# Performance work log

Measured on AMD Instinct MI355X. Metric: run time of the kernel, lower is better.

Reference implementation:

```python
import jax, jax.numpy as jnp
import numpy as np

B, S, H = 4, 2048, 1024
EXP_BITS, SIG_BITS = 5, 10  # rmode=1 -> round-to-nearest


def quantize(x):
    """Simulated low-precision float quantization (LightChop-style) with STE.

    exp_bits exponent bits (bias = 2^(e-1)-1, exponent clamped -> subnormal
    handling falls out of the clamp), sig_bits significand bits, round-to-nearest.
    """
    bias = 2 ** (EXP_BITS - 1) - 1
    ax = jnp.abs(x)
    e = jnp.floor(jnp.log2(jnp.where(ax > 0, ax, 1.0)))
    e = jnp.clip(e, 1 - bias, bias)               # clamp to representable exponent range
    scale = jnp.exp2(e - SIG_BITS)                # ulp at this exponent
    q = jnp.round(x / scale) * scale              # round significand to SIG_BITS bits
    max_val = (2.0 - 2.0 ** (-SIG_BITS)) * 2.0 ** bias
    q = jnp.clip(q, -max_val, max_val)            # saturate overflow
    # straight-through estimator: forward = q, backward = identity
    return x + jax.lax.stop_gradient(q - x)


def setup_inputs() -> dict:
    key = jax.random.key(0)
    ks = jax.random.split(key, 7)
    w_scale = 1.0 / np.sqrt(H)
    return {
        "x": jax.random.normal(ks[0], (B, S, H), dtype=jnp.float32),
        "Wq": jax.random.normal(ks[1], (H, H), dtype=jnp.float32) * w_scale,
        "bq": jax.random.normal(ks[2], (H,), dtype=jnp.float32) * 0.01,
        "Wk": jax.random.normal(ks[3], (H, H), dtype=jnp.float32) * w_scale,
        "bk": jax.random.normal(ks[4], (H,), dtype=jnp.float32) * 0.01,
        "Wv": jax.random.normal(ks[5], (H, H), dtype=jnp.float32) * w_scale,
        "bv": jax.random.normal(ks[6], (H,), dtype=jnp.float32) * 0.01,
    }


def reference(x, Wq, bq, Wk, bk, Wv, bv):
    # nn.Linear: y = x @ W.T + b   (W stored [out, in])
    q = quantize(jnp.einsum("bsh,oh->bso", x, Wq) + bq)
    k = quantize(jnp.einsum("bsh,oh->bso", x, Wk) + bk)
    v = quantize(jnp.einsum("bsh,oh->bso", x, Wv) + bv)
    inv_sqrt_h = 1.0 / (H ** 0.5)
    scores = quantize(jnp.einsum("bsh,bth->bst", q, k) * inv_sqrt_h)  # [B,S,S]
    attn = quantize(jax.nn.softmax(scores, axis=-1))
    return jnp.einsum("bst,bth->bsh", attn, v)
```

## Files before the change

kernel.cpp:

```cpp
#include <hip/hip_runtime.h>
#include <hip/hip_fp16.h>

#define B_ 4
#define S_ 2048
#define H_ 1024
#define M_ (B_ * S_)

typedef _Float16 f16;
typedef _Float16 f16x8 __attribute__((ext_vector_type(8)));
typedef _Float16 f16x4 __attribute__((ext_vector_type(4)));
typedef float f32x4 __attribute__((ext_vector_type(4)));

typedef __attribute__((address_space(3))) unsigned int* lds_u32p;
typedef const __attribute__((address_space(1))) unsigned int* gbl_u32p;

__device__ __forceinline__ void stage16(const f16* g, f16* l) {
  __builtin_amdgcn_global_load_lds((gbl_u32p)g, (lds_u32p)l, 16, 0, 0);
}

__global__ __launch_bounds__(256) void downconvert_all(
    const float* __restrict__ x, const float* __restrict__ W0,
    const float* __restrict__ W1, const float* __restrict__ W2,
    f16* __restrict__ xh, f16* __restrict__ Wh) {
  const int b = blockIdx.x;
  const float* src;
  f16* dst;
  long i;
  if (b < M_ * H_ / 1024) {
    src = x; dst = xh;
    i = (long)b * 256 + threadIdx.x;
  } else {
    const int wb = b - M_ * H_ / 1024;
    const int sel = wb >> 10;
    src = sel == 0 ? W0 : (sel == 1 ? W1 : W2);
    dst = Wh + (long)sel * H_ * H_;
    i = (long)(wb & 1023) * 256 + threadIdx.x;
  }
  f32x4 v = ((const f32x4*)src)[i];
  f16x4 h;
#pragma unroll
  for (int c = 0; c < 4; c++) h[c] = (f16)v[c];
  ((f16x4*)dst)[i] = h;
}

template <int KTOT, int EPI>
__global__ __launch_bounds__(256, 3)
void gemm_p(const f16* __restrict__ A, const f16* __restrict__ Bm,
            void* __restrict__ Cout, f16* __restrict__ vT,
            const float* __restrict__ bq, const float* __restrict__ bk,
            const float* __restrict__ bv,
            int lda, int ldb, int ldc, long sA, long sB, long sC,
            float alpha) {
  __shared__ __align__(16) f16 LA[3][128 * 32];
  __shared__ __align__(16) f16 LB[3][128 * 32];
  const int t = threadIdx.x;
  const int wave = t >> 6, lane = t & 63;
  const int quad = lane >> 4, l16 = lane & 15;
  const int wm = (wave & 1) * 64, wn = (wave >> 1) * 64;

  int sel = 0, ntile = 0, mtile = blockIdx.x * 128;
  const f16 *Ab, *Bb;
  if (EPI == 2) {
    sel = blockIdx.y >> 3;
    ntile = (blockIdx.y & 7) * 128;
    Ab = A + (long)mtile * lda;
    Bb = Bm + (long)sel * H_ * H_ + (long)ntile * ldb;
  } else {
    ntile = blockIdx.y * 128;
    Ab = A + blockIdx.z * sA + (long)mtile * lda;
    Bb = Bm + blockIdx.z * sB + (long)ntile * ldb;
  }

  const int srow = t >> 2;
  const int sch = (t & 3) ^ ((srow >> 1) & 3);
  const long ga = (long)srow * lda + sch * 8;
  const long gb = (long)srow * ldb + sch * 8;

  const int swz8 = (quad ^ ((l16 >> 1) & 3)) * 8;
  const int aoff = (wm + l16) * 32 + swz8;
  const int boff = (wn + l16) * 32 + swz8;

  f32x4 acc[4][4] = {};

#pragma unroll
  for (int p = 0; p < 2; ++p) {
    stage16(Ab + ga + p * 32,                    &LA[p][t * 8]);
    stage16(Ab + ga + (long)64 * lda + p * 32,   &LA[p][t * 8 + 2048]);
    stage16(Bb + gb + p * 32,                    &LB[p][t * 8]);
    stage16(Bb + gb + (long)64 * ldb + p * 32,   &LB[p][t * 8 + 2048]);
  }

  constexpr int NT = KTOT / 32;
  int rb = 0, sb = 2;
  long kg = 64;

#pragma unroll 3
  for (int kt = 0; kt < NT - 2; ++kt) {
    asm volatile("s_waitcnt vmcnt(4)" ::: "memory");
    __builtin_amdgcn_s_barrier();
    const f16* LAb = &LA[rb][0];
    const f16* LBb = &LB[rb][0];
    f16x8 af[4], bf[4];
#pragma unroll
    for (int i = 0; i < 4; ++i) {
      af[i] = *(const f16x8*)&LAb[aoff + i * 512];
      bf[i] = *(const f16x8*)&LBb[boff + i * 512];
    }
    f16* sa = &LA[sb][0];
    f16* sbb = &LB[sb][0];
    stage16(Ab + ga + kg,                  sa + t * 8);
    stage16(Ab + ga + (long)64 * lda + kg, sa + t * 8 + 2048);
    stage16(Bb + gb + kg,                  sbb + t * 8);
    stage16(Bb + gb + (long)64 * ldb + kg, sbb + t * 8 + 2048);
    __builtin_amdgcn_s_barrier();
    asm volatile("s_waitcnt lgkmcnt(0)" ::: "memory");
    __builtin_amdgcn_sched_barrier(0);
    __builtin_amdgcn_s_setprio(1);
#pragma unroll
    for (int i = 0; i < 4; ++i)
#pragma unroll
      for (int j = 0; j < 4; ++j)
        acc[i][j] = __builtin_amdgcn_mfma_f32_16x16x32_f16(af[i], bf[j],
                                                           acc[i][j], 0, 0, 0);
    __builtin_amdgcn_s_setprio(0);
    kg += 32;
    rb = rb == 2 ? 0 : rb + 1;
    sb = sb == 2 ? 0 : sb + 1;
  }

#pragma unroll
  for (int tp = 0; tp < 2; ++tp) {
    if (tp == 0)
      asm volatile("s_waitcnt vmcnt(4)" ::: "memory");
    else
      asm volatile("s_waitcnt vmcnt(0)" ::: "memory");
    __builtin_amdgcn_s_barrier();
    const f16* LAb = &LA[rb][0];
    const f16* LBb = &LB[rb][0];
    f16x8 af[4], bf[4];
#pragma unroll
    for (int i = 0; i < 4; ++i) {
      af[i] = *(const f16x8*)&LAb[aoff + i * 512];
      bf[i] = *(const f16x8*)&LBb[boff + i * 512];
    }
    __builtin_amdgcn_s_barrier();
    asm volatile("s_waitcnt lgkmcnt(0)" ::: "memory");
    __builtin_amdgcn_sched_barrier(0);
    __builtin_amdgcn_s_setprio(1);
#pragma unroll
    for (int i = 0; i < 4; ++i)
#pragma unroll
      for (int j = 0; j < 4; ++j)
        acc[i][j] = __builtin_amdgcn_mfma_f32_16x16x32_f16(af[i], bf[j],
                                                           acc[i][j], 0, 0, 0);
    __builtin_amdgcn_s_setprio(0);
    rb = rb == 2 ? 0 : rb + 1;
  }

  if (EPI == 0) {
    f16* C = (f16*)Cout + blockIdx.z * sC;
#pragma unroll
    for (int i = 0; i < 4; ++i)
#pragma unroll
      for (int j = 0; j < 4; ++j) {
        const long m = mtile + wm + i * 16 + quad * 4;
        const long n = ntile + wn + j * 16 + l16;
#pragma unroll
        for (int r = 0; r < 4; ++r)
          C[(m + r) * ldc + n] = (f16)(acc[i][j][r] * alpha);
      }
  } else if (EPI == 1) {
    float* C = (float*)Cout + blockIdx.z * sC;
#pragma unroll
    for (int i = 0; i < 4; ++i)
#pragma unroll
      for (int j = 0; j < 4; ++j) {
        const long m = mtile + wm + i * 16 + quad * 4;
        const long n = ntile + wn + j * 16 + l16;
#pragma unroll
        for (int r = 0; r < 4; ++r)
          C[(m + r) * ldc + n] = acc[i][j][r] * alpha;
      }
  } else {
    const float* bias = sel == 0 ? bq : (sel == 1 ? bk : bv);
    if (sel == 2) {
#pragma unroll
      for (int j = 0; j < 4; ++j) {
        const int n = ntile + wn + j * 16 + l16;
        const float bb = bias[n];
#pragma unroll
        for (int i = 0; i < 4; ++i) {
          const int m = mtile + wm + i * 16 + quad * 4;
          f16x4 pack;
#pragma unroll
          for (int r = 0; r < 4; ++r) pack[r] = (f16)(acc[i][j][r] + bb);
          *(f16x4*)&vT[((long)(m >> 11) * H_ + n) * S_ + (m & 2047)] = pack;
        }
      }
    } else {
      f16* C = (f16*)Cout + (long)sel * M_ * H_;
#pragma unroll
      for (int j = 0; j < 4; ++j) {
        const int n = ntile + wn + j * 16 + l16;
        const float bb = bias[n];
#pragma unroll
        for (int i = 0; i < 4; ++i) {
          const long m = mtile + wm + i * 16 + quad * 4;
#pragma unroll
          for (int r = 0; r < 4; ++r)
            C[(m + r) * ldc + n] = (f16)(acc[i][j][r] + bb);
        }
      }
    }
  }
}

__global__ __launch_bounds__(256) void softmax_q(f16* __restrict__ sc) {
  const long row = blockIdx.x;
  f16* p = sc + row * S_;
  const int t = threadIdx.x;
  const int wave = t >> 6, lane = t & 63;
  f16x8 v = ((const f16x8*)p)[t];
  float f[8];
  float m = -3.0e38f;
#pragma unroll
  for (int c = 0; c < 8; c++) { f[c] = (float)v[c]; m = fmaxf(m, f[c]); }
#pragma unroll
  for (int o = 32; o > 0; o >>= 1) m = fmaxf(m, __shfl_xor(m, o));
  __shared__ float redm[4], reds[4];
  if (lane == 0) redm[wave] = m;
  __syncthreads();
  m = fmaxf(fmaxf(redm[0], redm[1]), fmaxf(redm[2], redm[3]));
  float s = 0.f, e[8];
#pragma unroll
  for (int c = 0; c < 8; c++) { e[c] = __expf(f[c] - m); s += e[c]; }
#pragma unroll
  for (int o = 32; o > 0; o >>= 1) s += __shfl_xor(s, o);
  if (lane == 0) reds[wave] = s;
  __syncthreads();
  s = reds[0] + reds[1] + reds[2] + reds[3];
  float inv = 1.0f / s;
  f16x8 ov;
#pragma unroll
  for (int c = 0; c < 8; c++) ov[c] = (f16)(e[c] * inv);
  ((f16x8*)p)[t] = ov;
}

extern "C" void kernel_launch(void* const* d_in, const int* in_sizes, int n_in,
                              void* d_out, int out_size, void* d_ws, size_t ws_size,
                              hipStream_t stream) {
  (void)in_sizes; (void)n_in; (void)out_size; (void)ws_size;
  const float* x  = (const float*)d_in[0];
  const float* Wq = (const float*)d_in[1];
  const float* bq = (const float*)d_in[2];
  const float* Wk = (const float*)d_in[3];
  const float* bk = (const float*)d_in[4];
  const float* Wv = (const float*)d_in[5];
  const float* bv = (const float*)d_in[6];

  char* ws = (char*)d_ws;
  f16* xh  = (f16*)ws; ws += (size_t)M_ * H_ * 2;
  f16* Wh  = (f16*)ws; ws += (size_t)3 * H_ * H_ * 2;
  f16* qkv = (f16*)ws; ws += (size_t)2 * M_ * H_ * 2;
  f16* vT  = (f16*)ws; ws += (size_t)B_ * H_ * S_ * 2;
  f16* sc  = (f16*)ws; ws += (size_t)B_ * S_ * S_ * 2;

  downconvert_all<<<M_ * H_ / 1024 + 3 * H_ * H_ / 1024, 256, 0, stream>>>(
      x, Wq, Wk, Wv, xh, Wh);

  gemm_p<1024, 2><<<dim3(64, 24), 256, 0, stream>>>(
      xh, Wh, qkv, vT, bq, bk, bv, H_, H_, H_, 0, 0, 0, 0.f);

  gemm_p<1024, 0><<<dim3(16, 16, 4), 256, 0, stream>>>(
      qkv, qkv + (size_t)M_ * H_, sc, nullptr, nullptr, nullptr, nullptr,
      H_, H_, S_, (long)S_ * H_, (long)S_ * H_, (long)S_ * S_, 0.03125f);

  softmax_q<<<M_, 256, 0, stream>>>(sc);

  gemm_p<2048, 1><<<dim3(16, 8, 4), 256, 0, stream>>>(
      sc, vT, d_out, nullptr, nullptr, nullptr, nullptr,
      S_, S_, H_, (long)S_ * S_, (long)H_ * S_, (long)S_ * H_, 1.0f);
}
```

Baseline: 262.2 us.

## Switch GEMM to double-buffered 64-deep K tiles with one barrier per step

Replaces the three-stage, 32-deep K pipeline with a two-buffer scheme staging 64-deep K tiles, one barrier per tile and prefetch of the next tile during MFMA work on the current one. This cuts the number of barriers and wait points per K and gives larger LDS transfers per stage. In exchange, LDS use grows and occupancy hint drops from 3 to 2 blocks per CU, and each step waits for all outstanding loads, shortening the prefetch lead.

```diff
diff --git a/kernel.cpp b/kernel.cpp
--- a/kernel.cpp
+++ b/kernel.cpp
@@ -44,15 +44,15 @@
 }
 
 template <int KTOT, int EPI>
-__global__ __launch_bounds__(256, 3)
-void gemm_p(const f16* __restrict__ A, const f16* __restrict__ Bm,
+__global__ __launch_bounds__(256, 2)
+void gemm_d(const f16* __restrict__ A, const f16* __restrict__ Bm,
             void* __restrict__ Cout, f16* __restrict__ vT,
             const float* __restrict__ bq, const float* __restrict__ bk,
             const float* __restrict__ bv,
             int lda, int ldb, int ldc, long sA, long sB, long sC,
             float alpha) {
-  __shared__ __align__(16) f16 LA[3][128 * 32];
-  __shared__ __align__(16) f16 LB[3][128 * 32];
+  __shared__ __align__(16) f16 As[2][2 * 128 * 32];
+  __shared__ __align__(16) f16 Bs[2][2 * 128 * 32];
   const int t = threadIdx.x;
   const int wave = t >> 6, lane = t & 63;
   const int quad = lane >> 4, l16 = lane & 15;
@@ -82,80 +82,50 @@
 
   f32x4 acc[4][4] = {};
 
-#pragma unroll
-  for (int p = 0; p < 2; ++p) {
-    stage16(Ab + ga + p * 32,                    &LA[p][t * 8]);
-    stage16(Ab + ga + (long)64 * lda + p * 32,   &LA[p][t * 8 + 2048]);
-    stage16(Bb + gb + p * 32,                    &LB[p][t * 8]);
-    stage16(Bb + gb + (long)64 * ldb + p * 32,   &LB[p][t * 8 + 2048]);
-  }
-
-  constexpr int NT = KTOT / 32;
-  int rb = 0, sb = 2;
-  long kg = 64;
-
-#pragma unroll 3
-  for (int kt = 0; kt < NT - 2; ++kt) {
-    asm volatile("s_waitcnt vmcnt(4)" ::: "memory");
+#define STAGE_TILE(buf, k0)                                                  \
+  {                                                                          \
+    f16* sa_ = &As[buf][0];                                                  \
+    f16* sb_ = &Bs[buf][0];                                                  \
+    stage16(Ab + ga + (k0),                       sa_ + t * 8);              \
+    stage16(Ab + ga + (long)64 * lda + (k0),      sa_ + t * 8 + 2048);       \
+    stage16(Ab + ga + (k0) + 32,                  sa_ + t * 8 + 4096);       \
+    stage16(Ab + ga + (long)64 * lda + (k0) + 32, sa_ + t * 8 + 6144);       \
+    stage16(Bb + gb + (k0),                       sb_ + t * 8);              \
+    stage16(Bb + gb + (long)64 * ldb + (k0),      sb_ + t * 8 + 2048);       \
+    stage16(Bb + gb + (k0) + 32,                  sb_ + t * 8 + 4096);       \
+    stage16(Bb + gb + (long)64 * ldb + (k0) + 32, sb_ + t * 8 + 6144);       \
+  }
+
+  STAGE_TILE(0, 0)
+
+  constexpr int NT = KTOT / 64;
+#pragma unroll 2
+  for (int kt = 0; kt < NT; ++kt) {
+    const int cb = kt & 1;
+    asm volatile("s_waitcnt vmcnt(0)" ::: "memory");
     __builtin_amdgcn_s_barrier();
-    const f16* LAb = &LA[rb][0];
-    const f16* LBb = &LB[rb][0];
-    f16x8 af[4], bf[4];
-#pragma unroll
-    for (int i = 0; i < 4; ++i) {
-      af[i] = *(const f16x8*)&LAb[aoff + i * 512];
-      bf[i] = *(const f16x8*)&LBb[boff + i * 512];
+    if (kt + 1 < NT) {
+      STAGE_TILE(cb ^ 1, (kt + 1) * 64)
     }
-    f16* sa = &LA[sb][0];
-    f16* sbb = &LB[sb][0];
-    stage16(Ab + ga + kg,                  sa + t * 8);
-    stage16(Ab + ga + (long)64 * lda + kg, sa + t * 8 + 2048);
-    stage16(Bb + gb + kg,                  sbb + t * 8);
-    stage16(Bb + gb + (long)64 * ldb + kg, sbb + t * 8 + 2048);
-    __builtin_amdgcn_s_barrier();
-    asm volatile("s_waitcnt lgkmcnt(0)" ::: "memory");
-    __builtin_amdgcn_sched_barrier(0);
-    __builtin_amdgcn_s_setprio(1);
-#pragma unroll
-    for (int i = 0; i < 4; ++i)
-#pragma unroll
-      for (int j = 0; j < 4; ++j)
-        acc[i][j] = __builtin_amdgcn_mfma_f32_16x16x32_f16(af[i], bf[j],
-                                                           acc[i][j], 0, 0, 0);
-    __builtin_amdgcn_s_setprio(0);
-    kg += 32;
-    rb = rb == 2 ? 0 : rb + 1;
-    sb = sb == 2 ? 0 : sb + 1;
-  }
-
-#pragma unroll
-  for (int tp = 0; tp < 2; ++tp) {
-    if (tp == 0)
-      asm volatile("s_waitcnt vmcnt(4)" ::: "memory");
-    else
-      asm volatile("s_waitcnt vmcnt(0)" ::: "memory");
-    __builtin_amdgcn_s_barrier();
-    const f16* LAb = &LA[rb][0];
-    const f16* LBb = &LB[rb][0];
-    f16x8 af[4], bf[4];
-#pragma unroll
-    for (int i = 0; i < 4; ++i) {
-      af[i] = *(const f16x8*)&LAb[aoff + i * 512];
-      bf[i] = *(const f16x8*)&LBb[boff + i * 512];
+#pragma unroll
+    for (int kk = 0; kk < 2; ++kk) {
+      f16x8 af[4], bf[4];
+#pragma unroll
+      for (int i = 0; i < 4; ++i) {
+        af[i] = *(const f16x8*)&As[cb][kk * 4096 + aoff + i * 512];
+        bf[i] = *(const f16x8*)&Bs[cb][kk * 4096 + boff + i * 512];
+      }
+      __builtin_amdgcn_s_setprio(1);
+#pragma unroll
+      for (int i = 0; i < 4; ++i)
+#pragma unroll
+        for (int j = 0; j < 4; ++j)
+          acc[i][j] = __builtin_amdgcn_mfma_f32_16x16x32_f16(af[i], bf[j],
+                                                             acc[i][j], 0, 0, 0);
+      __builtin_amdgcn_s_setprio(0);
     }
-    __builtin_amdgcn_s_barrier();
-    asm volatile("s_waitcnt lgkmcnt(0)" ::: "memory");
-    __builtin_amdgcn_sched_barrier(0);
-    __builtin_amdgcn_s_setprio(1);
-#pragma unroll
-    for (int i = 0; i < 4; ++i)
-#pragma unroll
-      for (int j = 0; j < 4; ++j)
-        acc[i][j] = __builtin_amdgcn_mfma_f32_16x16x32_f16(af[i], bf[j],
-                                                           acc[i][j], 0, 0, 0);
-    __builtin_amdgcn_s_setprio(0);
-    rb = rb == 2 ? 0 : rb + 1;
-  }
+  }
+#undef STAGE_TILE
 
   if (EPI == 0) {
     f16* C = (f16*)Cout + blockIdx.z * sC;
@@ -268,16 +238,16 @@
   downconvert_all<<<M_ * H_ / 1024 + 3 * H_ * H_ / 1024, 256, 0, stream>>>(
       x, Wq, Wk, Wv, xh, Wh);
 
-  gemm_p<1024, 2><<<dim3(64, 24), 256, 0, stream>>>(
+  gemm_d<1024, 2><<<dim3(64, 24), 256, 0, stream>>>(
       xh, Wh, qkv, vT, bq, bk, bv, H_, H_, H_, 0, 0, 0, 0.f);
 
-  gemm_p<1024, 0><<<dim3(16, 16, 4), 256, 0, stream>>>(
+  gemm_d<1024, 0><<<dim3(16, 16, 4), 256, 0, stream>>>(
       qkv, qkv + (size_t)M_ * H_, sc, nullptr, nullptr, nullptr, nullptr,
       H_, H_, S_, (long)S_ * H_, (long)S_ * H_, (long)S_ * S_, 0.03125f);
 
   softmax_q<<<M_, 256, 0, stream>>>(sc);
 
-  gemm_p<2048, 1><<<dim3(16, 8, 4), 256, 0, stream>>>(
+  gemm_d<2048, 1><<<dim3(16, 8, 4), 256, 0, stream>>>(
       sc, vT, d_out, nullptr, nullptr, nullptr, nullptr,
       S_, S_, H_, (long)S_ * S_, (long)H_ * S_, (long)S_ * H_, 1.0f);
 }
```

After: 253.2 us. 1.04x faster.
